# Optimization experiments

Measured on AMD Instinct MI355X. Metric: run time of the kernel, lower is better.

The kernel has to match this reference:

```python
import jax, jax.numpy as jnp
import numpy as np

B, S, D, H = 2, 2048, 1024, 16
HD = D // H  # head_dim = 64


def setup_inputs() -> dict:
    key = jax.random.key(0)
    ks = jax.random.split(key, 7)
    s = 0.02
    return {
        "queries": jax.random.normal(ks[0], (B, S, D), jnp.float32),
        "keys": jax.random.normal(ks[1], (B, S, D), jnp.float32),
        "values": jax.random.normal(ks[2], (B, S, D), jnp.float32),
        "Wq": jax.random.normal(ks[3], (D, D), jnp.float32) * s,
        "Wk": jax.random.normal(ks[4], (D, D), jnp.float32) * s,
        "Wv": jax.random.normal(ks[5], (D, D), jnp.float32) * s,
        "Wo": jax.random.normal(ks[6], (D, D), jnp.float32) * s,
    }


def reference(queries, keys, values, Wq, Wk, Wv, Wo):
    # Projections (torch Linear: x @ W.T); split into heads -> [B, H, S, HD]
    def split_heads(x):
        b, s, _ = x.shape
        return x.reshape(b, s, H, HD).transpose(0, 2, 1, 3)

    q = split_heads(queries @ Wq.T)
    k = split_heads(keys @ Wk.T)
    v = split_heads(values @ Wv.T)

    scale = 1.0 / jnp.sqrt(jnp.asarray(HD, q.dtype))
    scores = jnp.einsum("bhqd,bhkd->bhqk", q, k) * scale  # [B,H,S,S]
    attn = jax.nn.softmax(scores, axis=-1)
    ctx = jnp.einsum("bhqk,bhkd->bhqd", attn, v)  # [B,H,S,HD]
    out = ctx.transpose(0, 2, 1, 3).reshape(queries.shape[0], -1, D)
    return out @ Wo.T
```

## Files before the change

kernel.cpp:

```cpp
#include <hip/hip_runtime.h>
#include <hip/hip_bf16.h>


#define B_ 2
#define S_ 2048
#define D_ 1024
#define H_ 16
#define HD_ 64
#define NE_ (B_ * S_ * D_)
#define WN_ (D_ * D_)

typedef unsigned short u16;
typedef unsigned int u32;
typedef u16 __attribute__((may_alias)) u16_ma;
typedef float __attribute__((may_alias)) f32_ma;
typedef u32 v4u __attribute__((ext_vector_type(4)));
typedef v4u __attribute__((may_alias)) v4u_ma;
typedef short bf16x8 __attribute__((ext_vector_type(8)));
typedef bf16x8 __attribute__((may_alias)) bf16x8_ma;
typedef float f32x4 __attribute__((ext_vector_type(4)));
typedef float f32x16 __attribute__((ext_vector_type(16)));

__device__ __forceinline__ float bf2f(u16 u) {
  u32 x = ((u32)u) << 16;
  return __builtin_bit_cast(float, x);
}
__device__ __forceinline__ u16 f2bf(float f) {
  __hip_bfloat16 h = __float2bfloat16(f);
  return __builtin_bit_cast(u16, h);
}
__device__ __forceinline__ u32 pk2(u32 alo, u32 ahi) {
  return (u32)f2bf(__builtin_bit_cast(float, alo)) |
         ((u32)f2bf(__builtin_bit_cast(float, ahi)) << 16);
}
__device__ __forceinline__ u32 pkf(float lo, float hi) {
  return (u32)f2bf(lo) | ((u32)f2bf(hi) << 16);
}

__device__ __forceinline__ void gl_lds16(const u16* g, u16* l) {
  auto gp = (const __attribute__((address_space(1))) unsigned int*)(const void*)g;
  auto lp = (__attribute__((address_space(3))) unsigned int*)(void*)l;
  __builtin_amdgcn_global_load_lds(gp, lp, 16, 0, 0);
}

__device__ __forceinline__ bool detect_f32(const u16* Wg) {
  const int lane = threadIdx.x & 63;
  bool hit = false;
#pragma unroll
  for (int i = 0; i < 4; ++i) {
    v4u u = *(const v4u_ma*)(Wg + lane * 32 + i * 8);
#pragma unroll
    for (int j = 0; j < 4; ++j) {
      u32 w = u[j];
      hit |= (((w >> 7) & 0xFFu) >= 0xF0u) || (((w >> 23) & 0xFFu) >= 0xF0u);
    }
  }
  return __any(hit);
}

__global__ __launch_bounds__(256) void convert_bf16(
    const void* s0, const void* s1, const void* s2, const void* s3,
    const void* s4, const void* s5, const void* s6, u16* __restrict__ dst_in,
    u16* __restrict__ dst_w, const u16* __restrict__ Wdet) {
  const bool det = detect_f32(Wdet);
  const int y = blockIdx.y;
  const void* src;
  u16* dst;
  int n;
  if (y < 3) {
    src = (y == 0) ? s0 : ((y == 1) ? s1 : s2);
    dst = dst_in + (size_t)y * NE_;
    n = NE_;
  } else {
    src = (y == 3) ? s3 : ((y == 4) ? s4 : ((y == 5) ? s5 : s6));
    dst = dst_w + (size_t)(y - 3) * WN_;
    n = WN_;
  }
  const int i = (blockIdx.x * 256 + threadIdx.x) * 8;
  if (i >= n) return;
  v4u out;
  if (det) {
    const v4u_ma* fp = (const v4u_ma*)((const float*)src + i);
    v4u f0 = fp[0], f1 = fp[1];
    out[0] = pk2(f0[0], f0[1]);
    out[1] = pk2(f0[2], f0[3]);
    out[2] = pk2(f1[0], f1[1]);
    out[3] = pk2(f1[2], f1[3]);
  } else {
    out = *(const v4u_ma*)((const u16*)src + i);
  }
  *(v4u_ma*)(dst + i) = out;
}

template <int BN, bool OUT_DET>
__global__ __launch_bounds__(256) void proj_g(
    const u16* __restrict__ Ab, const u16* __restrict__ Wb,
    void* __restrict__ Cb, const u16* __restrict__ Wdet) {
  __shared__ u16 Al[128 * 64];
  __shared__ u16 Wl[BN * 64];

  const bool outf32 = OUT_DET ? detect_f32(Wdet) : false;

  const int tid = threadIdx.x;
  const int lane = tid & 63, wid = tid >> 6;
  const int lg = lane >> 4, li = lane & 15;
  const int wr = wid >> 1, wc = wid & 1;
  const int z = blockIdx.z;
  const char* Ag = (const char*)(Ab + (size_t)z * NE_);
  const char* Wg = (const char*)(Wb + (size_t)z * WN_);
  const int m0 = blockIdx.x * 128, n0 = blockIdx.y * BN;

  const int lr = lane >> 3;
  const int swzb = ((lane & 7) * 16) ^ (lr << 4);

  constexpr int NF = BN / 32;
  f32x4 acc[4][NF];
#pragma unroll
  for (int m = 0; m < 4; ++m)
#pragma unroll
    for (int n = 0; n < NF; ++n) acc[m][n] = (f32x4){0.f, 0.f, 0.f, 0.f};

  for (int kt = 0; kt < 16; ++kt) {
    const int k0b = kt * 128;
    __syncthreads();
#pragma unroll
    for (int c = 0; c < 4; ++c) {
      const int row = wid * 32 + c * 8 + lr;
      gl_lds16((const u16*)(Ag + (size_t)(m0 + row) * 2048 + k0b + swzb),
               Al + (wid * 32 + c * 8) * 64);
    }
    if constexpr (BN == 128) {
#pragma unroll
      for (int c = 0; c < 4; ++c) {
        const int row = wid * 32 + c * 8 + lr;
        gl_lds16((const u16*)(Wg + (size_t)(n0 + row) * 2048 + k0b + swzb),
                 Wl + (wid * 32 + c * 8) * 64);
      }
    } else {
#pragma unroll
      for (int c = 0; c < 2; ++c) {
        const int row = wid * 16 + c * 8 + lr;
        gl_lds16((const u16*)(Wg + (size_t)(n0 + row) * 2048 + k0b + swzb),
                 Wl + (wid * 16 + c * 8) * 64);
      }
    }
    __syncthreads();

#pragma unroll
    for (int ks = 0; ks < 2; ++ks) {
      bf16x8 af[4], bw[NF];
#pragma unroll
      for (int m = 0; m < 4; ++m) {
        const int row = wr * 64 + m * 16 + li;
        af[m] = *(const bf16x8_ma*)((const char*)Al + row * 128 +
                                    ((ks * 64 + lg * 16) ^ ((row & 7) << 4)));
      }
#pragma unroll
      for (int n = 0; n < NF; ++n) {
        const int row = wc * (BN / 2) + n * 16 + li;
        bw[n] = *(const bf16x8_ma*)((const char*)Wl + row * 128 +
                                    ((ks * 64 + lg * 16) ^ ((row & 7) << 4)));
      }
#pragma unroll
      for (int m = 0; m < 4; ++m)
#pragma unroll
        for (int n = 0; n < NF; ++n)
          acc[m][n] = __builtin_amdgcn_mfma_f32_16x16x32_bf16(af[m], bw[n],
                                                              acc[m][n], 0, 0, 0);
    }
  }

  const float zs = (!OUT_DET && z == 0) ? 0.125f : 1.0f;
#pragma unroll
  for (int m = 0; m < 4; ++m)
#pragma unroll
    for (int n = 0; n < NF; ++n)
#pragma unroll
      for (int r = 0; r < 4; ++r) {
        const int row = m0 + wr * 64 + m * 16 + lg * 4 + r;
        const int col = n0 + wc * (BN / 2) + n * 16 + li;
        const size_t idx = (size_t)row * D_ + col;
        const float v = acc[m][n][r] * zs;
        if (OUT_DET) {
          if (outf32)
            ((f32_ma*)Cb)[idx] = v;
          else
            ((u16_ma*)Cb)[idx] = f2bf(v);
        } else {
          ((u16_ma*)((u16*)Cb + (size_t)z * NE_))[idx] = f2bf(v);
        }
      }
}

__global__ __launch_bounds__(256) void attn3(
    const u16* __restrict__ Qg, const u16* __restrict__ Kg,
    const u16* __restrict__ Vg, u16* __restrict__ Og) {
  __shared__ u16 Kl[64 * 64];
  __shared__ u16 VTl[64 * 64];

  const int tid = threadIdx.x;
  const int wid = tid >> 6, lane = tid & 63;
  const int l31 = lane & 31;
  const int hi = lane >> 5;

  const int bid = blockIdx.x;
  const int swz = (bid & 7) * 64 + (bid >> 3);
  const int qb = swz & 15;
  const int h = (swz >> 4) & 15;
  const int b = swz >> 8;
  const size_t bbase = (size_t)b * S_ * D_;
  const int hoff = h * HD_;
  const int q0w = qb * 128 + wid * 32;

  bf16x8 bq[4];
  {
    const u16* qp = Qg + bbase + (size_t)(q0w + l31) * D_ + hoff + hi * 8;
#pragma unroll
    for (int dblk = 0; dblk < 4; ++dblk)
      bq[dblk] = *(const bf16x8_ma*)(qp + dblk * 16);
  }

  f32x16 o0, o1;
#pragma unroll
  for (int i = 0; i < 16; ++i) {
    o0[i] = 0.f;
    o1[i] = 0.f;
  }
  float mrun = -1e30f, lrun = 0.f;

  const int krr = tid >> 3;
  const int kc8 = (tid & 7) * 8;
  const int vkr = lane;
  const int vd0 = wid * 8;

  v4u kr0, kr1, vr0, vr1;
  auto kv_load = [&](int kt) {
    const int key0 = kt * 64;
    kr0 = *(const v4u_ma*)(Kg + bbase + (size_t)(key0 + krr) * D_ + hoff + kc8);
    kr1 = *(const v4u_ma*)(Kg + bbase + (size_t)(key0 + 32 + krr) * D_ + hoff + kc8);
    vr0 = *(const v4u_ma*)(Vg + bbase + (size_t)(key0 + vkr) * D_ + hoff + vd0);
    vr1 = *(const v4u_ma*)(Vg + bbase + (size_t)(key0 + vkr) * D_ + hoff + vd0 + 32);
  };
  auto kv_write = [&]() {
    const int ksw = (krr & 7) << 4;
    *(v4u_ma*)((char*)Kl + krr * 128 + ((kc8 * 2) ^ ksw)) = kr0;
    *(v4u_ma*)((char*)Kl + (32 + krr) * 128 + ((kc8 * 2) ^ ksw)) = kr1;
    union {
      v4u v;
      u16 e[8];
    } uu;
    uu.v = vr0;
#pragma unroll
    for (int j = 0; j < 8; ++j) {
      const int d = vd0 + j;
      *(u16*)((char*)VTl + d * 128 + ((vkr * 2) ^ ((d & 7) << 4))) = uu.e[j];
    }
    uu.v = vr1;
#pragma unroll
    for (int j = 0; j < 8; ++j) {
      const int d = vd0 + 32 + j;
      *(u16*)((char*)VTl + d * 128 + ((vkr * 2) ^ ((d & 7) << 4))) = uu.e[j];
    }
  };

  kv_load(0);
  kv_write();

  const int swk = (l31 & 7) << 4;

  for (int kt = 0; kt < S_ / 64; ++kt) {
    __syncthreads();
    if (kt < S_ / 64 - 1) kv_load(kt + 1);

    f32x16 sT0, sT1;
#pragma unroll
    for (int i = 0; i < 16; ++i) {
      sT0[i] = 0.f;
      sT1[i] = 0.f;
    }
    __builtin_amdgcn_s_setprio(1);
#pragma unroll
    for (int dblk = 0; dblk < 4; ++dblk) {
      const int cb = (dblk * 32 + hi * 16);
      bf16x8 a0 = *(const bf16x8_ma*)((const char*)Kl + l31 * 128 + (cb ^ swk));
      bf16x8 a1 =
          *(const bf16x8_ma*)((const char*)Kl + (32 + l31) * 128 + (cb ^ swk));
      sT0 = __builtin_amdgcn_mfma_f32_32x32x16_bf16(a0, bq[dblk], sT0, 0, 0, 0);
      sT1 = __builtin_amdgcn_mfma_f32_32x32x16_bf16(a1, bq[dblk], sT1, 0, 0, 0);
    }
    __builtin_amdgcn_s_setprio(0);

    float pmax = sT0[0];
#pragma unroll
    for (int i = 1; i < 16; ++i) pmax = fmaxf(pmax, sT0[i]);
#pragma unroll
    for (int i = 0; i < 16; ++i) pmax = fmaxf(pmax, sT1[i]);
    pmax = fmaxf(pmax, __shfl_xor(pmax, 32));
    if (!__all(pmax - mrun <= 8.f)) {
      const float mnew = fmaxf(mrun, pmax);
      const float al = __expf(mrun - mnew);
      mrun = mnew;
      lrun *= al;
      o0 *= al;
      o1 *= al;
    }

    u32 w[16];
    float sum = 0.f;
#pragma unroll
    for (int kh = 0; kh < 2; ++kh)
#pragma unroll
      for (int g = 0; g < 4; ++g)
#pragma unroll
        for (int u = 0; u < 2; ++u) {
          const int r = g * 4 + 2 * u;
          const float pe =
              __expf((kh ? sT1[r] : sT0[r]) - mrun);
          const float po =
              __expf((kh ? sT1[r + 1] : sT0[r + 1]) - mrun);
          sum += pe + po;
          w[kh * 8 + g * 2 + u] = pkf(pe, po);
        }
    sum += __shfl_xor(sum, 32);
    lrun += sum;

    bf16x8 pf[4];
#pragma unroll
    for (int km = 0; km < 4; ++km) {
      const int a = 4 * km;
      const u32 s0 = hi ? w[a] : w[a + 2];
      const u32 s1 = hi ? w[a + 1] : w[a + 3];
      const u32 r0 = (u32)__shfl_xor((int)s0, 32);
      const u32 r1 = (u32)__shfl_xor((int)s1, 32);
      union {
        u32 d[4];
        bf16x8 v;
      } uu;
      uu.d[0] = hi ? r0 : w[a];
      uu.d[1] = hi ? r1 : w[a + 1];
      uu.d[2] = hi ? w[a + 2] : r0;
      uu.d[3] = hi ? w[a + 3] : r1;
      pf[km] = uu.v;
    }

    __builtin_amdgcn_s_setprio(1);
#pragma unroll
    for (int km = 0; km < 4; ++km) {
      const int cb = (km * 32 + hi * 16);
      bf16x8 v0 = *(const bf16x8_ma*)((const char*)VTl + l31 * 128 + (cb ^ swk));
      bf16x8 v1 =
          *(const bf16x8_ma*)((const char*)VTl + (32 + l31) * 128 + (cb ^ swk));
      o0 = __builtin_amdgcn_mfma_f32_32x32x16_bf16(v0, pf[km], o0, 0, 0, 0);
      o1 = __builtin_amdgcn_mfma_f32_32x32x16_bf16(v1, pf[km], o1, 0, 0, 0);
    }
    __builtin_amdgcn_s_setprio(0);

    __syncthreads();
    if (kt < S_ / 64 - 1) kv_write();
  }

  const float inv = 1.f / lrun;
  u16* orow = Og + bbase + (size_t)(q0w + l31) * D_ + hoff;
#pragma unroll
  for (int r = 0; r < 16; ++r) {
    const int d0 = (r & 3) + 8 * (r >> 2) + 4 * hi;
    orow[d0] = f2bf(o0[r] * inv);
    orow[d0 + 32] = f2bf(o1[r] * inv);
  }
}

template <bool A_SCR, bool SCR_F32, bool OUT_FINAL>
__global__ __launch_bounds__(256) void proj_slow(
    const void* __restrict__ Ag, const u16* __restrict__ Wg,
    void* __restrict__ Cg) {
  const bool det = detect_f32(Wg);
  const bool a_f32 = A_SCR ? SCR_F32 : det;
  const int m = blockIdx.x;
  const int n = blockIdx.y * 256 + threadIdx.x;
  const size_t arow = (size_t)m * D_;
  const size_t wrow = (size_t)n * D_;
  float acc = 0.f;
  for (int k = 0; k < D_; ++k) {
    float a = a_f32 ? ((const f32_ma*)Ag)[arow + k]
                    : bf2f(((const u16_ma*)Ag)[arow + k]);
    float w = det ? ((const f32_ma*)Wg)[wrow + k]
                  : bf2f(((const u16_ma*)Wg)[wrow + k]);
    acc += a * w;
  }
  const size_t ci = (size_t)m * D_ + n;
  const bool c_f32 = OUT_FINAL ? det : SCR_F32;
  if (c_f32)
    ((f32_ma*)Cg)[ci] = acc;
  else
    ((u16_ma*)Cg)[ci] = f2bf(acc);
}

template <bool SCR_F32>
__global__ __launch_bounds__(256) void attn_slow(
    const void* __restrict__ Qg, const void* __restrict__ Kg,
    const void* __restrict__ Vg, void* __restrict__ Cg) {
  const int tid = threadIdx.x;
  const int qblk = blockIdx.x & 7;
  const int h = (blockIdx.x >> 3) & 15;
  const int b = blockIdx.x >> 7;
  const int q = qblk * 256 + tid;
  const size_t base = (size_t)b * S_ * D_;
  const int hoff = h * HD_;
  float qv[64];
  {
    const size_t qrow = base + (size_t)q * D_ + hoff;
    for (int d = 0; d < 64; ++d)
      qv[d] = SCR_F32 ? ((const f32_ma*)Qg)[qrow + d]
                      : bf2f(((const u16_ma*)Qg)[qrow + d]);
  }
  float o[64];
  for (int d = 0; d < 64; ++d) o[d] = 0.f;
  float m = -1e30f, l = 0.f;
  for (int key = 0; key < S_; ++key) {
    const size_t krow = base + (size_t)key * D_ + hoff;
    float s = 0.f;
    for (int d = 0; d < 64; ++d) {
      float kx = SCR_F32 ? ((const f32_ma*)Kg)[krow + d]
                         : bf2f(((const u16_ma*)Kg)[krow + d]);
      s += qv[d] * kx;
    }
    s *= 0.125f;
    float mn = fmaxf(m, s);
    float al = expf(m - mn);
    float pe = expf(s - mn);
    m = mn;
    l = l * al + pe;
    for (int d = 0; d < 64; ++d) {
      float vx = SCR_F32 ? ((const f32_ma*)Vg)[krow + d]
                         : bf2f(((const u16_ma*)Vg)[krow + d]);
      o[d] = o[d] * al + pe * vx;
    }
  }
  const float il = 1.f / l;
  const size_t crow = base + (size_t)q * D_ + hoff;
  for (int d = 0; d < 64; ++d) {
    if (SCR_F32)
      ((f32_ma*)Cg)[crow + d] = o[d] * il;
    else
      ((u16_ma*)Cg)[crow + d] = f2bf(o[d] * il);
  }
}

extern "C" void kernel_launch(void* const* d_in, const int* in_sizes, int n_in,
                              void* d_out, int out_size, void* d_ws,
                              size_t ws_size, hipStream_t stream) {
  const u16* Wdet = (const u16*)d_in[3];
  dim3 blk(256);

  if (ws_size >= (size_t)4 * NE_ * sizeof(float)) {
    u16* Qi = (u16*)d_ws;
    u16* Wc = Qi + (size_t)3 * NE_;
    u16* Qp = Wc + (size_t)4 * WN_;
    u16* Xp = Qp + (size_t)3 * NE_;

    convert_bf16<<<dim3(2048, 7), blk, 0, stream>>>(
        d_in[0], d_in[1], d_in[2], d_in[3], d_in[4], d_in[5], d_in[6], Qi, Wc,
        Wdet);
    proj_g<128, false><<<dim3(32, 8, 3), blk, 0, stream>>>(Qi, Wc, Qp, Wdet);
    attn3<<<dim3(512), blk, 0, stream>>>(Qp, Qp + NE_, Qp + (size_t)2 * NE_, Xp);
    proj_g<64, true><<<dim3(32, 16, 1), blk, 0, stream>>>(
        Xp, Wc + (size_t)3 * WN_, d_out, Wdet);
  } else {
    dim3 gproj(B_ * S_, D_ / 256);
    dim3 gattn(B_ * H_ * (S_ / 256));
    u16* Qp = (u16*)d_out;
    u16* Kp = (u16*)d_in[0];
    u16* Vp = (u16*)d_in[1];
    u16* Xp = (u16*)d_in[2];
    proj_slow<false, false, false><<<gproj, blk, 0, stream>>>(
        d_in[0], (const u16*)d_in[3], Qp);
    proj_slow<false, false, false><<<gproj, blk, 0, stream>>>(
        d_in[1], (const u16*)d_in[4], Kp);
    proj_slow<false, false, false><<<gproj, blk, 0, stream>>>(
        d_in[2], (const u16*)d_in[5], Vp);
    attn_slow<false><<<gattn, blk, 0, stream>>>(Qp, Kp, Vp, Xp);
    proj_slow<true, false, true><<<gproj, blk, 0, stream>>>(
        Xp, (const u16*)d_in[6], d_out);
  }
}
```

Before: 228.9 us.

## Double-buffer K/V shared tiles in attention to drop second barrier

```diff
diff --git a/kernel.cpp b/kernel.cpp
--- a/kernel.cpp
+++ b/kernel.cpp
@@ -195,8 +195,8 @@
 __global__ __launch_bounds__(256) void attn3(
     const u16* __restrict__ Qg, const u16* __restrict__ Kg,
     const u16* __restrict__ Vg, u16* __restrict__ Og) {
-  __shared__ u16 Kl[64 * 64];
-  __shared__ u16 VTl[64 * 64];
+  __shared__ u16 Kl[2][64 * 64];
+  __shared__ u16 VTl[2][64 * 64];
 
   const int tid = threadIdx.x;
   const int wid = tid >> 6, lane = tid & 63;
@@ -241,10 +241,12 @@
     vr0 = *(const v4u_ma*)(Vg + bbase + (size_t)(key0 + vkr) * D_ + hoff + vd0);
     vr1 = *(const v4u_ma*)(Vg + bbase + (size_t)(key0 + vkr) * D_ + hoff + vd0 + 32);
   };
-  auto kv_write = [&]() {
+  auto kv_write = [&](int bi) {
+    char* Kb = (char*)&Kl[bi][0];
+    char* Vb = (char*)&VTl[bi][0];
     const int ksw = (krr & 7) << 4;
-    *(v4u_ma*)((char*)Kl + krr * 128 + ((kc8 * 2) ^ ksw)) = kr0;
-    *(v4u_ma*)((char*)Kl + (32 + krr) * 128 + ((kc8 * 2) ^ ksw)) = kr1;
+    *(v4u_ma*)(Kb + krr * 128 + ((kc8 * 2) ^ ksw)) = kr0;
+    *(v4u_ma*)(Kb + (32 + krr) * 128 + ((kc8 * 2) ^ ksw)) = kr1;
     union {
       v4u v;
       u16 e[8];
@@ -253,18 +255,18 @@
 #pragma unroll
     for (int j = 0; j < 8; ++j) {
       const int d = vd0 + j;
-      *(u16*)((char*)VTl + d * 128 + ((vkr * 2) ^ ((d & 7) << 4))) = uu.e[j];
+      *(u16*)(Vb + d * 128 + ((vkr * 2) ^ ((d & 7) << 4))) = uu.e[j];
     }
     uu.v = vr1;
 #pragma unroll
     for (int j = 0; j < 8; ++j) {
       const int d = vd0 + 32 + j;
-      *(u16*)((char*)VTl + d * 128 + ((vkr * 2) ^ ((d & 7) << 4))) = uu.e[j];
+      *(u16*)(Vb + d * 128 + ((vkr * 2) ^ ((d & 7) << 4))) = uu.e[j];
     }
   };
 
   kv_load(0);
-  kv_write();
+  kv_write(0);
 
   const int swk = (l31 & 7) << 4;
 
@@ -272,6 +274,9 @@
     __syncthreads();
     if (kt < S_ / 64 - 1) kv_load(kt + 1);
 
+    const char* Kb = (const char*)&Kl[kt & 1][0];
+    const char* Vb = (const char*)&VTl[kt & 1][0];
+
     f32x16 sT0, sT1;
 #pragma unroll
     for (int i = 0; i < 16; ++i) {
@@ -282,9 +287,8 @@
 #pragma unroll
     for (int dblk = 0; dblk < 4; ++dblk) {
       const int cb = (dblk * 32 + hi * 16);
-      bf16x8 a0 = *(const bf16x8_ma*)((const char*)Kl + l31 * 128 + (cb ^ swk));
-      bf16x8 a1 =
-          *(const bf16x8_ma*)((const char*)Kl + (32 + l31) * 128 + (cb ^ swk));
+      bf16x8 a0 = *(const bf16x8_ma*)(Kb + l31 * 128 + (cb ^ swk));
+      bf16x8 a1 = *(const bf16x8_ma*)(Kb + (32 + l31) * 128 + (cb ^ swk));
       sT0 = __builtin_amdgcn_mfma_f32_32x32x16_bf16(a0, bq[dblk], sT0, 0, 0, 0);
       sT1 = __builtin_amdgcn_mfma_f32_32x32x16_bf16(a1, bq[dblk], sT1, 0, 0, 0);
     }
@@ -292,11 +296,14 @@
 
     float pmax = sT0[0];
 #pragma unroll
-    for (int i = 1; i < 16; ++i) pmax = fmaxf(pmax, sT0[i]);
-#pragma unroll
-    for (int i = 0; i < 16; ++i) pmax = fmaxf(pmax, sT1[i]);
+    for (int i = 0; i < 7; ++i)
+      pmax = fmaxf(fmaxf(pmax, sT0[2 * i + 1]), sT0[2 * i + 2]);
+    pmax = fmaxf(pmax, sT0[15]);
+#pragma unroll
+    for (int i = 0; i < 8; ++i)
+      pmax = fmaxf(fmaxf(pmax, sT1[2 * i]), sT1[2 * i + 1]);
     pmax = fmaxf(pmax, __shfl_xor(pmax, 32));
-    if (!__all(pmax - mrun <= 8.f)) {
+    if (!__all(pmax - mrun <= 8.0f)) {
       const float mnew = fmaxf(mrun, pmax);
       const float al = __expf(mrun - mnew);
       mrun = mnew;
@@ -314,10 +321,8 @@
 #pragma unroll
         for (int u = 0; u < 2; ++u) {
           const int r = g * 4 + 2 * u;
-          const float pe =
-              __expf((kh ? sT1[r] : sT0[r]) - mrun);
-          const float po =
-              __expf((kh ? sT1[r + 1] : sT0[r + 1]) - mrun);
+          const float pe = __expf((kh ? sT1[r] : sT0[r]) - mrun);
+          const float po = __expf((kh ? sT1[r + 1] : sT0[r + 1]) - mrun);
           sum += pe + po;
           w[kh * 8 + g * 2 + u] = pkf(pe, po);
         }
@@ -347,16 +352,14 @@
 #pragma unroll
     for (int km = 0; km < 4; ++km) {
       const int cb = (km * 32 + hi * 16);
-      bf16x8 v0 = *(const bf16x8_ma*)((const char*)VTl + l31 * 128 + (cb ^ swk));
-      bf16x8 v1 =
-          *(const bf16x8_ma*)((const char*)VTl + (32 + l31) * 128 + (cb ^ swk));
+      bf16x8 v0 = *(const bf16x8_ma*)(Vb + l31 * 128 + (cb ^ swk));
+      bf16x8 v1 = *(const bf16x8_ma*)(Vb + (32 + l31) * 128 + (cb ^ swk));
       o0 = __builtin_amdgcn_mfma_f32_32x32x16_bf16(v0, pf[km], o0, 0, 0, 0);
       o1 = __builtin_amdgcn_mfma_f32_32x32x16_bf16(v1, pf[km], o1, 0, 0, 0);
     }
     __builtin_amdgcn_s_setprio(0);
 
-    __syncthreads();
-    if (kt < S_ / 64 - 1) kv_write();
+    if (kt < S_ / 64 - 1) kv_write((kt + 1) & 1);
   }
 
   const float inv = 1.f / lrun;
```

Result: no change. 232.3 us (+1.5%).
